# Optimization experiments

Measured on AMD Instinct MI355X. Metric: run time of the kernel, lower is better.

The kernel has to match this reference:

```python
import jax, jax.numpy as jnp
import numpy as np

G_DOWNSAMPLED = 16  # g_downsampled_dimension: tiling factor
XF_DIM = 1024       # xf_dimension
BATCH = 2048


def setup_inputs() -> dict:
    key = jax.random.key(0)
    k1, k2 = jax.random.split(key)
    xf = jax.random.normal(k1, (BATCH, XF_DIM), dtype=jnp.float32)
    wp = jax.random.normal(k2, (1,), dtype=jnp.float32)
    return {"xf": xf, "wp": wp}


def reference(xf, wp):
    # xf_r = relu(xf - mean_batch(xf))
    xf_r = jax.nn.relu(xf - jnp.mean(xf, axis=0))
    # fn_xf = (xf_r - mean(xf_r)) / std(xf_r), std unbiased (torch default ddof=1)
    mu = jnp.mean(xf_r, axis=0)
    sd = jnp.std(xf_r, axis=0, ddof=1)
    fn_xf = (xf_r - mu) / sd
    # matmul with W_tile = kron(ones(1,g), eye(xf_dim)) is an exact tile along features
    x_ = wp * jnp.tile(fn_xf, (1, G_DOWNSAMPLED))  # [batch, g*xf_dim]
    return x_
```

## Files before the change

kernel.cpp:

```cpp
#include <hip/hip_runtime.h>

#define BATCH 2048
#define FDIM  1024
#define GTILE 16
#define F4    (FDIM / 4)
#define CHUNKS 128
#define ROWS_PER_CHUNK (BATCH / CHUNKS)

#define OFF_P1   0
#define OFF_P2S  131072
#define OFF_P2Q  262144
#define OFF_MEAN 393216
#define OFF_SC   394240
#define OFF_CC   395264

__device__ __forceinline__ void v4add(float4& a, const float4& b) {
    a.x += b.x; a.y += b.y; a.z += b.z; a.w += b.w;
}

__global__ void k1_partial_sum(const float4* __restrict__ xf, float4* __restrict__ p1) {
    const int tid = threadIdx.x;
    const int chunk = blockIdx.x;
    const float4* p = xf + (size_t)chunk * ROWS_PER_CHUNK * F4 + tid;
    float4 s = {0.f, 0.f, 0.f, 0.f};
#pragma unroll
    for (int r = 0; r < ROWS_PER_CHUNK; ++r) v4add(s, p[r * F4]);
    p1[chunk * F4 + tid] = s;
}

__global__ void k2_relu_partial(const float4* __restrict__ xf,
                                const float4* __restrict__ p1,
                                float4* __restrict__ p2s,
                                float4* __restrict__ p2q) {
    const int tid = threadIdx.x;
    const int chunk = blockIdx.x;
    float4 m = {0.f, 0.f, 0.f, 0.f};
#pragma unroll 8
    for (int c = 0; c < CHUNKS; ++c) v4add(m, p1[c * F4 + tid]);
    const float inv_n = 1.0f / (float)BATCH;
    m.x *= inv_n; m.y *= inv_n; m.z *= inv_n; m.w *= inv_n;

    const float4* p = xf + (size_t)chunk * ROWS_PER_CHUNK * F4 + tid;
    float4 s = {0.f, 0.f, 0.f, 0.f};
    float4 q = {0.f, 0.f, 0.f, 0.f};
#pragma unroll
    for (int r = 0; r < ROWS_PER_CHUNK; ++r) {
        float4 v = p[r * F4];
        float rx = fmaxf(v.x - m.x, 0.f);
        float ry = fmaxf(v.y - m.y, 0.f);
        float rz = fmaxf(v.z - m.z, 0.f);
        float rw = fmaxf(v.w - m.w, 0.f);
        s.x += rx; s.y += ry; s.z += rz; s.w += rw;
        q.x += rx * rx; q.y += ry * ry; q.z += rz * rz; q.w += rw * rw;
    }
    p2s[chunk * F4 + tid] = s;
    p2q[chunk * F4 + tid] = q;
}

__global__ void k3_finalize(const float* __restrict__ wp,
                            const float4* __restrict__ p1,
                            const float4* __restrict__ p2s,
                            const float4* __restrict__ p2q,
                            float4* __restrict__ mean,
                            float4* __restrict__ sc,
                            float4* __restrict__ cc) {
    __shared__ float4 rm[256], rs[256], rq[256];
    const int t = threadIdx.x;
    const int b = blockIdx.x;
    const int cg = b * 16 + (t & 15);
    const int slice = t >> 4;
    const int c0 = slice * (CHUNKS / 16);
    float4 m = {0.f,0.f,0.f,0.f}, s = {0.f,0.f,0.f,0.f}, q = {0.f,0.f,0.f,0.f};
#pragma unroll
    for (int c = c0; c < c0 + CHUNKS / 16; ++c) {
        v4add(m, p1[c * F4 + cg]);
        v4add(s, p2s[c * F4 + cg]);
        v4add(q, p2q[c * F4 + cg]);
    }
    rm[t] = m; rs[t] = s; rq[t] = q;
    __syncthreads();
    for (int off = 128; off >= 16; off >>= 1) {
        if (t < off) { v4add(rm[t], rm[t + off]); v4add(rs[t], rs[t + off]); v4add(rq[t], rq[t + off]); }
        __syncthreads();
    }
    if (t < 16) {
        const float inv_n = 1.0f / (float)BATCH;
        const float w = wp[0];
        float4 M = rm[t], S = rs[t], Q = rq[t];
        float4 mn, scale, cmb;
        float mu, var;
        mn.x = M.x * inv_n;
        mu = S.x * inv_n; var = (Q.x - S.x * mu) / (float)(BATCH - 1);
        scale.x = w * rsqrtf(var); cmb.x = mu * scale.x;
        mn.y = M.y * inv_n;
        mu = S.y * inv_n; var = (Q.y - S.y * mu) / (float)(BATCH - 1);
        scale.y = w * rsqrtf(var); cmb.y = mu * scale.y;
        mn.z = M.z * inv_n;
        mu = S.z * inv_n; var = (Q.z - S.z * mu) / (float)(BATCH - 1);
        scale.z = w * rsqrtf(var); cmb.z = mu * scale.z;
        mn.w = M.w * inv_n;
        mu = S.w * inv_n; var = (Q.w - S.w * mu) / (float)(BATCH - 1);
        scale.w = w * rsqrtf(var); cmb.w = mu * scale.w;
        mean[b * 16 + t] = mn;
        sc[b * 16 + t]   = scale;
        cc[b * 16 + t]   = cmb;
    }
}

__global__ void __launch_bounds__(256) k4_write(const float4* __restrict__ xf,
                                                const float4* __restrict__ mean,
                                                const float4* __restrict__ sc,
                                                const float4* __restrict__ cc,
                                                float4* __restrict__ out) {
    const int tid = threadIdx.x;
    const int row0 = blockIdx.x * 2;
    float4 v0 = xf[(size_t)row0 * F4 + tid];
    float4 v1 = xf[(size_t)(row0 + 1) * F4 + tid];
    float4 m = mean[tid];
    float4 a = sc[tid];
    float4 c = cc[tid];
    float4 o0, o1;
    o0.x = fmaxf(v0.x - m.x, 0.f) * a.x - c.x;
    o0.y = fmaxf(v0.y - m.y, 0.f) * a.y - c.y;
    o0.z = fmaxf(v0.z - m.z, 0.f) * a.z - c.z;
    o0.w = fmaxf(v0.w - m.w, 0.f) * a.w - c.w;
    o1.x = fmaxf(v1.x - m.x, 0.f) * a.x - c.x;
    o1.y = fmaxf(v1.y - m.y, 0.f) * a.y - c.y;
    o1.z = fmaxf(v1.z - m.z, 0.f) * a.z - c.z;
    o1.w = fmaxf(v1.w - m.w, 0.f) * a.w - c.w;
    float4* dst0 = out + (size_t)row0 * (GTILE * F4) + tid;
    float4* dst1 = dst0 + (GTILE * F4);
#pragma unroll
    for (int g = 0; g < GTILE; ++g) {
        dst0[g * F4] = o0;
        dst1[g * F4] = o1;
    }
}

extern "C" void kernel_launch(void* const* d_in, const int* in_sizes, int n_in,
                              void* d_out, int out_size, void* d_ws, size_t ws_size,
                              hipStream_t stream) {
    const float4* xf4 = (const float4*)d_in[0];
    const float* wp = (const float*)d_in[1];
    float* ws = (float*)d_ws;
    float4* out = (float4*)d_out;

    float4* p1   = (float4*)(ws + OFF_P1);
    float4* p2s  = (float4*)(ws + OFF_P2S);
    float4* p2q  = (float4*)(ws + OFF_P2Q);
    float4* mean = (float4*)(ws + OFF_MEAN);
    float4* sc   = (float4*)(ws + OFF_SC);
    float4* cc   = (float4*)(ws + OFF_CC);

    k1_partial_sum<<<CHUNKS, 256, 0, stream>>>(xf4, p1);
    k2_relu_partial<<<CHUNKS, 256, 0, stream>>>(xf4, p1, p2s, p2q);
    k3_finalize<<<16, 256, 0, stream>>>(wp, p1, p2s, p2q, mean, sc, cc);
    k4_write<<<BATCH / 2, 256, 0, stream>>>(xf4, mean, sc, cc, out);
}
```

Baseline: 154.5 us.

## Replace partial-sum buffers and finalize kernel with atomic reductions and nontemporal stores

Column statistics are now accumulated with float atomicAdd into small zeroed workspace arrays, using 256 blocks of 8 rows instead of 128 chunk partials followed by a separate finalize kernel. The per-column scale and offset are recomputed inside the write kernel, and the 16x tiled output is written with nontemporal stores. This drops one kernel launch and the partial-buffer reads, in exchange for a memset, atomic contention on 1024 addresses and nondeterministic summation order.

```diff
diff --git a/kernel.cpp b/kernel.cpp
--- a/kernel.cpp
+++ b/kernel.cpp
@@ -4,47 +4,47 @@
 #define FDIM  1024
 #define GTILE 16
 #define F4    (FDIM / 4)
-#define CHUNKS 128
-#define ROWS_PER_CHUNK (BATCH / CHUNKS)
+#define RA    8
+#define NBLK  (BATCH / RA)
 
-#define OFF_P1   0
-#define OFF_P2S  131072
-#define OFF_P2Q  262144
-#define OFF_MEAN 393216
-#define OFF_SC   394240
-#define OFF_CC   395264
+#define OFF_CS 0
+#define OFF_S  1024
+#define OFF_Q  2048
 
-__device__ __forceinline__ void v4add(float4& a, const float4& b) {
-    a.x += b.x; a.y += b.y; a.z += b.z; a.w += b.w;
+typedef float v4f __attribute__((ext_vector_type(4)));
+
+__global__ void __launch_bounds__(256) ka_colsum(const float4* __restrict__ xf,
+                                                 float* __restrict__ colsum) {
+    const int tid = threadIdx.x;
+    const int b   = blockIdx.x;
+    const float4* p = xf + (size_t)b * RA * F4 + tid;
+    float4 s = {0.f, 0.f, 0.f, 0.f};
+#pragma unroll
+    for (int r = 0; r < RA; ++r) {
+        float4 v = p[r * F4];
+        s.x += v.x; s.y += v.y; s.z += v.z; s.w += v.w;
+    }
+    atomicAdd(&colsum[tid * 4 + 0], s.x);
+    atomicAdd(&colsum[tid * 4 + 1], s.y);
+    atomicAdd(&colsum[tid * 4 + 2], s.z);
+    atomicAdd(&colsum[tid * 4 + 3], s.w);
 }
 
-__global__ void k1_partial_sum(const float4* __restrict__ xf, float4* __restrict__ p1) {
+__global__ void __launch_bounds__(256) kb_relustats(const float4* __restrict__ xf,
+                                                    const float4* __restrict__ colsum4,
+                                                    float* __restrict__ ssum,
+                                                    float* __restrict__ sq) {
     const int tid = threadIdx.x;
-    const int chunk = blockIdx.x;
-    const float4* p = xf + (size_t)chunk * ROWS_PER_CHUNK * F4 + tid;
-    float4 s = {0.f, 0.f, 0.f, 0.f};
-#pragma unroll
-    for (int r = 0; r < ROWS_PER_CHUNK; ++r) v4add(s, p[r * F4]);
-    p1[chunk * F4 + tid] = s;
-}
-
-__global__ void k2_relu_partial(const float4* __restrict__ xf,
-                                const float4* __restrict__ p1,
-                                float4* __restrict__ p2s,
-                                float4* __restrict__ p2q) {
-    const int tid = threadIdx.x;
-    const int chunk = blockIdx.x;
-    float4 m = {0.f, 0.f, 0.f, 0.f};
-#pragma unroll 8
-    for (int c = 0; c < CHUNKS; ++c) v4add(m, p1[c * F4 + tid]);
+    const int b   = blockIdx.x;
     const float inv_n = 1.0f / (float)BATCH;
+    float4 m = colsum4[tid];
     m.x *= inv_n; m.y *= inv_n; m.z *= inv_n; m.w *= inv_n;
 
-    const float4* p = xf + (size_t)chunk * ROWS_PER_CHUNK * F4 + tid;
+    const float4* p = xf + (size_t)b * RA * F4 + tid;
     float4 s = {0.f, 0.f, 0.f, 0.f};
     float4 q = {0.f, 0.f, 0.f, 0.f};
 #pragma unroll
-    for (int r = 0; r < ROWS_PER_CHUNK; ++r) {
+    for (int r = 0; r < RA; ++r) {
         float4 v = p[r * F4];
         float rx = fmaxf(v.x - m.x, 0.f);
         float ry = fmaxf(v.y - m.y, 0.f);
@@ -53,87 +53,62 @@
         s.x += rx; s.y += ry; s.z += rz; s.w += rw;
         q.x += rx * rx; q.y += ry * ry; q.z += rz * rz; q.w += rw * rw;
     }
-    p2s[chunk * F4 + tid] = s;
-    p2q[chunk * F4 + tid] = q;
+    atomicAdd(&ssum[tid * 4 + 0], s.x);
+    atomicAdd(&ssum[tid * 4 + 1], s.y);
+    atomicAdd(&ssum[tid * 4 + 2], s.z);
+    atomicAdd(&ssum[tid * 4 + 3], s.w);
+    atomicAdd(&sq[tid * 4 + 0], q.x);
+    atomicAdd(&sq[tid * 4 + 1], q.y);
+    atomicAdd(&sq[tid * 4 + 2], q.z);
+    atomicAdd(&sq[tid * 4 + 3], q.w);
 }
 
-__global__ void k3_finalize(const float* __restrict__ wp,
-                            const float4* __restrict__ p1,
-                            const float4* __restrict__ p2s,
-                            const float4* __restrict__ p2q,
-                            float4* __restrict__ mean,
-                            float4* __restrict__ sc,
-                            float4* __restrict__ cc) {
-    __shared__ float4 rm[256], rs[256], rq[256];
-    const int t = threadIdx.x;
-    const int b = blockIdx.x;
-    const int cg = b * 16 + (t & 15);
-    const int slice = t >> 4;
-    const int c0 = slice * (CHUNKS / 16);
-    float4 m = {0.f,0.f,0.f,0.f}, s = {0.f,0.f,0.f,0.f}, q = {0.f,0.f,0.f,0.f};
-#pragma unroll
-    for (int c = c0; c < c0 + CHUNKS / 16; ++c) {
-        v4add(m, p1[c * F4 + cg]);
-        v4add(s, p2s[c * F4 + cg]);
-        v4add(q, p2q[c * F4 + cg]);
-    }
-    rm[t] = m; rs[t] = s; rq[t] = q;
-    __syncthreads();
-    for (int off = 128; off >= 16; off >>= 1) {
-        if (t < off) { v4add(rm[t], rm[t + off]); v4add(rs[t], rs[t + off]); v4add(rq[t], rq[t + off]); }
-        __syncthreads();
-    }
-    if (t < 16) {
-        const float inv_n = 1.0f / (float)BATCH;
-        const float w = wp[0];
-        float4 M = rm[t], S = rs[t], Q = rq[t];
-        float4 mn, scale, cmb;
-        float mu, var;
-        mn.x = M.x * inv_n;
-        mu = S.x * inv_n; var = (Q.x - S.x * mu) / (float)(BATCH - 1);
-        scale.x = w * rsqrtf(var); cmb.x = mu * scale.x;
-        mn.y = M.y * inv_n;
-        mu = S.y * inv_n; var = (Q.y - S.y * mu) / (float)(BATCH - 1);
-        scale.y = w * rsqrtf(var); cmb.y = mu * scale.y;
-        mn.z = M.z * inv_n;
-        mu = S.z * inv_n; var = (Q.z - S.z * mu) / (float)(BATCH - 1);
-        scale.z = w * rsqrtf(var); cmb.z = mu * scale.z;
-        mn.w = M.w * inv_n;
-        mu = S.w * inv_n; var = (Q.w - S.w * mu) / (float)(BATCH - 1);
-        scale.w = w * rsqrtf(var); cmb.w = mu * scale.w;
-        mean[b * 16 + t] = mn;
-        sc[b * 16 + t]   = scale;
-        cc[b * 16 + t]   = cmb;
-    }
-}
+__global__ void __launch_bounds__(256) kd_write(const float4* __restrict__ xf,
+                                                const float* __restrict__ wp,
+                                                const float4* __restrict__ colsum4,
+                                                const float4* __restrict__ ssum4,
+                                                const float4* __restrict__ sq4,
+                                                float4* __restrict__ out) {
+    const int tid  = threadIdx.x;
+    const int row0 = blockIdx.x * 2;
+    const float inv_n  = 1.0f / (float)BATCH;
+    const float inv_n1 = 1.0f / (float)(BATCH - 1);
+    const float w = wp[0];
 
-__global__ void __launch_bounds__(256) k4_write(const float4* __restrict__ xf,
-                                                const float4* __restrict__ mean,
-                                                const float4* __restrict__ sc,
-                                                const float4* __restrict__ cc,
-                                                float4* __restrict__ out) {
-    const int tid = threadIdx.x;
-    const int row0 = blockIdx.x * 2;
+    float4 M = colsum4[tid];
+    float4 S = ssum4[tid];
+    float4 Q = sq4[tid];
+
+    float4 m, scale, cc;
+    float mu;
+    m.x = M.x * inv_n;
+    mu = S.x * inv_n; scale.x = w * rsqrtf((Q.x - S.x * mu) * inv_n1); cc.x = mu * scale.x;
+    m.y = M.y * inv_n;
+    mu = S.y * inv_n; scale.y = w * rsqrtf((Q.y - S.y * mu) * inv_n1); cc.y = mu * scale.y;
+    m.z = M.z * inv_n;
+    mu = S.z * inv_n; scale.z = w * rsqrtf((Q.z - S.z * mu) * inv_n1); cc.z = mu * scale.z;
+    m.w = M.w * inv_n;
+    mu = S.w * inv_n; scale.w = w * rsqrtf((Q.w - S.w * mu) * inv_n1); cc.w = mu * scale.w;
+
     float4 v0 = xf[(size_t)row0 * F4 + tid];
     float4 v1 = xf[(size_t)(row0 + 1) * F4 + tid];
-    float4 m = mean[tid];
-    float4 a = sc[tid];
-    float4 c = cc[tid];
-    float4 o0, o1;
-    o0.x = fmaxf(v0.x - m.x, 0.f) * a.x - c.x;
-    o0.y = fmaxf(v0.y - m.y, 0.f) * a.y - c.y;
-    o0.z = fmaxf(v0.z - m.z, 0.f) * a.z - c.z;
-    o0.w = fmaxf(v0.w - m.w, 0.f) * a.w - c.w;
-    o1.x = fmaxf(v1.x - m.x, 0.f) * a.x - c.x;
-    o1.y = fmaxf(v1.y - m.y, 0.f) * a.y - c.y;
-    o1.z = fmaxf(v1.z - m.z, 0.f) * a.z - c.z;
-    o1.w = fmaxf(v1.w - m.w, 0.f) * a.w - c.w;
-    float4* dst0 = out + (size_t)row0 * (GTILE * F4) + tid;
-    float4* dst1 = dst0 + (GTILE * F4);
+
+    v4f o0, o1;
+    o0.x = fmaxf(v0.x - m.x, 0.f) * scale.x - cc.x;
+    o0.y = fmaxf(v0.y - m.y, 0.f) * scale.y - cc.y;
+    o0.z = fmaxf(v0.z - m.z, 0.f) * scale.z - cc.z;
+    o0.w = fmaxf(v0.w - m.w, 0.f) * scale.w - cc.w;
+    o1.x = fmaxf(v1.x - m.x, 0.f) * scale.x - cc.x;
+    o1.y = fmaxf(v1.y - m.y, 0.f) * scale.y - cc.y;
+    o1.z = fmaxf(v1.z - m.z, 0.f) * scale.z - cc.z;
+    o1.w = fmaxf(v1.w - m.w, 0.f) * scale.w - cc.w;
+
+    v4f* dst0 = (v4f*)(out + (size_t)row0 * (GTILE * F4) + tid);
+    v4f* dst1 = dst0 + (GTILE * F4);
 #pragma unroll
     for (int g = 0; g < GTILE; ++g) {
-        dst0[g * F4] = o0;
-        dst1[g * F4] = o1;
+        __builtin_nontemporal_store(o0, dst0 + g * F4);
+        __builtin_nontemporal_store(o1, dst1 + g * F4);
     }
 }
 
@@ -141,19 +116,17 @@
                               void* d_out, int out_size, void* d_ws, size_t ws_size,
                               hipStream_t stream) {
     const float4* xf4 = (const float4*)d_in[0];
-    const float* wp = (const float*)d_in[1];
+    const float* wp   = (const float*)d_in[1];
     float* ws = (float*)d_ws;
-    float4* out = (float4*)d_out;
+    float* colsum = ws + OFF_CS;
+    float* ssum   = ws + OFF_S;
+    float* sq     = ws + OFF_Q;
 
-    float4* p1   = (float4*)(ws + OFF_P1);
-    float4* p2s  = (float4*)(ws + OFF_P2S);
-    float4* p2q  = (float4*)(ws + OFF_P2Q);
-    float4* mean = (float4*)(ws + OFF_MEAN);
-    float4* sc   = (float4*)(ws + OFF_SC);
-    float4* cc   = (float4*)(ws + OFF_CC);
+    (void)hipMemsetAsync(d_ws, 0, 3 * 1024 * sizeof(float), stream);
 
-    k1_partial_sum<<<CHUNKS, 256, 0, stream>>>(xf4, p1);
-    k2_relu_partial<<<CHUNKS, 256, 0, stream>>>(xf4, p1, p2s, p2q);
-    k3_finalize<<<16, 256, 0, stream>>>(wp, p1, p2s, p2q, mean, sc, cc);
-    k4_write<<<BATCH / 2, 256, 0, stream>>>(xf4, mean, sc, cc, out);
+    ka_colsum<<<NBLK, 256, 0, stream>>>(xf4, colsum);
+    kb_relustats<<<NBLK, 256, 0, stream>>>(xf4, (const float4*)colsum, ssum, sq);
+    kd_write<<<BATCH / 2, 256, 0, stream>>>(xf4, wp, (const float4*)colsum,
+                                            (const float4*)ssum, (const float4*)sq,
+                                            (float4*)d_out);
 }
```

Result: slower. 210.1 us (+36.0%).

## Split reductions into more blocks, add mean kernel, use nontemporal output stores

Applied to the files above, without the earlier changes.

Doubles the number of row-chunk blocks in both statistics passes (8 rows per block instead of 16), giving more parallelism over the 256+ CUs. A separate k_mean kernel finalizes the column mean once, so the second pass no longer re-reduces all partials in every block. The finalize kernel is restructured to scalar columns over 64 partials per quarter-block. The 128MB output write now uses nontemporal stores to avoid cache pollution. The cost is one extra kernel launch.

```diff
diff --git a/kernel.cpp b/kernel.cpp
--- a/kernel.cpp
+++ b/kernel.cpp
@@ -3,48 +3,62 @@
 #define BATCH 2048
 #define FDIM  1024
 #define GTILE 16
-#define F4    (FDIM / 4)
-#define CHUNKS 128
-#define ROWS_PER_CHUNK (BATCH / CHUNKS)
+#define F4    256
+#define NB1   256
+#define RA    8
 
 #define OFF_P1   0
-#define OFF_P2S  131072
-#define OFF_P2Q  262144
-#define OFF_MEAN 393216
-#define OFF_SC   394240
-#define OFF_CC   395264
+#define OFF_P2S  262144
+#define OFF_P2Q  524288
+#define OFF_MEAN 786432
+#define OFF_SC   787456
+#define OFF_CC   788480
+
+typedef float v4f __attribute__((ext_vector_type(4)));
 
 __device__ __forceinline__ void v4add(float4& a, const float4& b) {
     a.x += b.x; a.y += b.y; a.z += b.z; a.w += b.w;
 }
 
-__global__ void k1_partial_sum(const float4* __restrict__ xf, float4* __restrict__ p1) {
-    const int tid = threadIdx.x;
-    const int chunk = blockIdx.x;
-    const float4* p = xf + (size_t)chunk * ROWS_PER_CHUNK * F4 + tid;
+__global__ void __launch_bounds__(256) k1_colsum(const float4* __restrict__ xf,
+                                                 float4* __restrict__ p1) {
+    const int cg = threadIdx.x;
+    const int b  = blockIdx.x;
+    const float4* p = xf + (size_t)b * RA * F4 + cg;
     float4 s = {0.f, 0.f, 0.f, 0.f};
 #pragma unroll
-    for (int r = 0; r < ROWS_PER_CHUNK; ++r) v4add(s, p[r * F4]);
-    p1[chunk * F4 + tid] = s;
+    for (int r = 0; r < RA; ++r) v4add(s, p[r * F4]);
+    p1[b * F4 + cg] = s;
 }
 
-__global__ void k2_relu_partial(const float4* __restrict__ xf,
-                                const float4* __restrict__ p1,
-                                float4* __restrict__ p2s,
-                                float4* __restrict__ p2q) {
-    const int tid = threadIdx.x;
-    const int chunk = blockIdx.x;
-    float4 m = {0.f, 0.f, 0.f, 0.f};
+__global__ void __launch_bounds__(256) k_mean(const float* __restrict__ p1,
+                                              float* __restrict__ mean) {
+    __shared__ float sm[256];
+    const int t   = threadIdx.x;
+    const int b   = blockIdx.x;
+    const int col = b * 64 + (t & 63);
+    const int q   = t >> 6;
+    float s = 0.f;
 #pragma unroll 8
-    for (int c = 0; c < CHUNKS; ++c) v4add(m, p1[c * F4 + tid]);
-    const float inv_n = 1.0f / (float)BATCH;
-    m.x *= inv_n; m.y *= inv_n; m.z *= inv_n; m.w *= inv_n;
+    for (int k = 0; k < 64; ++k) s += p1[(q * 64 + k) * FDIM + col];
+    sm[t] = s;
+    __syncthreads();
+    if (t < 64)
+        mean[col] = (sm[t] + sm[t + 64] + sm[t + 128] + sm[t + 192]) * (1.0f / (float)BATCH);
+}
 
-    const float4* p = xf + (size_t)chunk * ROWS_PER_CHUNK * F4 + tid;
+__global__ void __launch_bounds__(256) k2_relustats(const float4* __restrict__ xf,
+                                                    const float4* __restrict__ mean4,
+                                                    float4* __restrict__ p2s,
+                                                    float4* __restrict__ p2q) {
+    const int cg = threadIdx.x;
+    const int b  = blockIdx.x;
+    float4 m = mean4[cg];
+    const float4* p = xf + (size_t)b * RA * F4 + cg;
     float4 s = {0.f, 0.f, 0.f, 0.f};
     float4 q = {0.f, 0.f, 0.f, 0.f};
 #pragma unroll
-    for (int r = 0; r < ROWS_PER_CHUNK; ++r) {
+    for (int r = 0; r < RA; ++r) {
         float4 v = p[r * F4];
         float rx = fmaxf(v.x - m.x, 0.f);
         float ry = fmaxf(v.y - m.y, 0.f);
@@ -53,57 +67,39 @@
         s.x += rx; s.y += ry; s.z += rz; s.w += rw;
         q.x += rx * rx; q.y += ry * ry; q.z += rz * rz; q.w += rw * rw;
     }
-    p2s[chunk * F4 + tid] = s;
-    p2q[chunk * F4 + tid] = q;
+    p2s[b * F4 + cg] = s;
+    p2q[b * F4 + cg] = q;
 }
 
-__global__ void k3_finalize(const float* __restrict__ wp,
-                            const float4* __restrict__ p1,
-                            const float4* __restrict__ p2s,
-                            const float4* __restrict__ p2q,
-                            float4* __restrict__ mean,
-                            float4* __restrict__ sc,
-                            float4* __restrict__ cc) {
-    __shared__ float4 rm[256], rs[256], rq[256];
-    const int t = threadIdx.x;
-    const int b = blockIdx.x;
-    const int cg = b * 16 + (t & 15);
-    const int slice = t >> 4;
-    const int c0 = slice * (CHUNKS / 16);
-    float4 m = {0.f,0.f,0.f,0.f}, s = {0.f,0.f,0.f,0.f}, q = {0.f,0.f,0.f,0.f};
-#pragma unroll
-    for (int c = c0; c < c0 + CHUNKS / 16; ++c) {
-        v4add(m, p1[c * F4 + cg]);
-        v4add(s, p2s[c * F4 + cg]);
-        v4add(q, p2q[c * F4 + cg]);
+__global__ void __launch_bounds__(256) k3_scale(const float* __restrict__ wp,
+                                                const float* __restrict__ p2s,
+                                                const float* __restrict__ p2q,
+                                                float* __restrict__ sc,
+                                                float* __restrict__ cc) {
+    __shared__ float ss[256];
+    __shared__ float sq[256];
+    const int t   = threadIdx.x;
+    const int b   = blockIdx.x;
+    const int col = b * 64 + (t & 63);
+    const int q   = t >> 6;
+    float S = 0.f, Q = 0.f;
+#pragma unroll 8
+    for (int k = 0; k < 64; ++k) {
+        const int r = q * 64 + k;
+        S += p2s[r * FDIM + col];
+        Q += p2q[r * FDIM + col];
     }
-    rm[t] = m; rs[t] = s; rq[t] = q;
+    ss[t] = S; sq[t] = Q;
     __syncthreads();
-    for (int off = 128; off >= 16; off >>= 1) {
-        if (t < off) { v4add(rm[t], rm[t + off]); v4add(rs[t], rs[t + off]); v4add(rq[t], rq[t + off]); }
-        __syncthreads();
-    }
-    if (t < 16) {
-        const float inv_n = 1.0f / (float)BATCH;
-        const float w = wp[0];
-        float4 M = rm[t], S = rs[t], Q = rq[t];
-        float4 mn, scale, cmb;
-        float mu, var;
-        mn.x = M.x * inv_n;
-        mu = S.x * inv_n; var = (Q.x - S.x * mu) / (float)(BATCH - 1);
-        scale.x = w * rsqrtf(var); cmb.x = mu * scale.x;
-        mn.y = M.y * inv_n;
-        mu = S.y * inv_n; var = (Q.y - S.y * mu) / (float)(BATCH - 1);
-        scale.y = w * rsqrtf(var); cmb.y = mu * scale.y;
-        mn.z = M.z * inv_n;
-        mu = S.z * inv_n; var = (Q.z - S.z * mu) / (float)(BATCH - 1);
-        scale.z = w * rsqrtf(var); cmb.z = mu * scale.z;
-        mn.w = M.w * inv_n;
-        mu = S.w * inv_n; var = (Q.w - S.w * mu) / (float)(BATCH - 1);
-        scale.w = w * rsqrtf(var); cmb.w = mu * scale.w;
-        mean[b * 16 + t] = mn;
-        sc[b * 16 + t]   = scale;
-        cc[b * 16 + t]   = cmb;
+    if (t < 64) {
+        S = ss[t] + ss[t + 64] + ss[t + 128] + ss[t + 192];
+        Q = sq[t] + sq[t + 64] + sq[t + 128] + sq[t + 192];
+        const float w   = wp[0];
+        const float mu  = S * (1.0f / (float)BATCH);
+        const float var = (Q - S * mu) * (1.0f / (float)(BATCH - 1));
+        const float scale = w * rsqrtf(var);
+        sc[col] = scale;
+        cc[col] = mu * scale;
     }
 }
 
@@ -112,14 +108,14 @@
                                                 const float4* __restrict__ sc,
                                                 const float4* __restrict__ cc,
                                                 float4* __restrict__ out) {
-    const int tid = threadIdx.x;
+    const int tid  = threadIdx.x;
     const int row0 = blockIdx.x * 2;
     float4 v0 = xf[(size_t)row0 * F4 + tid];
     float4 v1 = xf[(size_t)(row0 + 1) * F4 + tid];
     float4 m = mean[tid];
     float4 a = sc[tid];
     float4 c = cc[tid];
-    float4 o0, o1;
+    v4f o0, o1;
     o0.x = fmaxf(v0.x - m.x, 0.f) * a.x - c.x;
     o0.y = fmaxf(v0.y - m.y, 0.f) * a.y - c.y;
     o0.z = fmaxf(v0.z - m.z, 0.f) * a.z - c.z;
@@ -128,12 +124,12 @@
     o1.y = fmaxf(v1.y - m.y, 0.f) * a.y - c.y;
     o1.z = fmaxf(v1.z - m.z, 0.f) * a.z - c.z;
     o1.w = fmaxf(v1.w - m.w, 0.f) * a.w - c.w;
-    float4* dst0 = out + (size_t)row0 * (GTILE * F4) + tid;
-    float4* dst1 = dst0 + (GTILE * F4);
+    v4f* dst0 = (v4f*)(out + (size_t)row0 * (GTILE * F4) + tid);
+    v4f* dst1 = dst0 + (GTILE * F4);
 #pragma unroll
     for (int g = 0; g < GTILE; ++g) {
-        dst0[g * F4] = o0;
-        dst1[g * F4] = o1;
+        __builtin_nontemporal_store(o0, dst0 + g * F4);
+        __builtin_nontemporal_store(o1, dst1 + g * F4);
     }
 }
 
@@ -141,19 +137,21 @@
                               void* d_out, int out_size, void* d_ws, size_t ws_size,
                               hipStream_t stream) {
     const float4* xf4 = (const float4*)d_in[0];
-    const float* wp = (const float*)d_in[1];
+    const float* wp   = (const float*)d_in[1];
     float* ws = (float*)d_ws;
-    float4* out = (float4*)d_out;
 
     float4* p1   = (float4*)(ws + OFF_P1);
     float4* p2s  = (float4*)(ws + OFF_P2S);
     float4* p2q  = (float4*)(ws + OFF_P2Q);
-    float4* mean = (float4*)(ws + OFF_MEAN);
-    float4* sc   = (float4*)(ws + OFF_SC);
-    float4* cc   = (float4*)(ws + OFF_CC);
+    float*  mean = ws + OFF_MEAN;
+    float*  sc   = ws + OFF_SC;
+    float*  cc   = ws + OFF_CC;
 
-    k1_partial_sum<<<CHUNKS, 256, 0, stream>>>(xf4, p1);
-    k2_relu_partial<<<CHUNKS, 256, 0, stream>>>(xf4, p1, p2s, p2q);
-    k3_finalize<<<16, 256, 0, stream>>>(wp, p1, p2s, p2q, mean, sc, cc);
-    k4_write<<<BATCH / 2, 256, 0, stream>>>(xf4, mean, sc, cc, out);
+    k1_colsum  <<<NB1, 256, 0, stream>>>(xf4, p1);
+    k_mean     <<<16,  256, 0, stream>>>((const float*)p1, mean);
+    k2_relustats<<<NB1, 256, 0, stream>>>(xf4, (const float4*)mean, p2s, p2q);
+    k3_scale   <<<16,  256, 0, stream>>>(wp, (const float*)p2s, (const float*)p2q, sc, cc);
+    k4_write   <<<BATCH / 2, 256, 0, stream>>>(xf4, (const float4*)mean,
+                                               (const float4*)sc, (const float4*)cc,
+                                               (float4*)d_out);
 }
```

Result: slower. 158.6 us (+2.6%).
